# Optimization experiments

Hardware: AMD Instinct MI355X
Metric: run time of the kernel (lower is better)

The kernel has to match this reference:

```python
import jax, jax.numpy as jnp
import numpy as np

B, S, D = 8, 1024, 1024
H, K = 16, 64  # num_heads, key_dim
NEG_INF = -1e9  # Keras _large_compatible_negative for float32


def setup_inputs() -> dict:
    key = jax.random.key(0)
    ks = jax.random.split(key, 10)
    x = jax.random.normal(ks[0], (B, S, D), dtype=jnp.float32)
    mask = jax.random.bernoulli(ks[1], 0.9, (B, S))  # bool per-token mask
    w = lambda k, shp: (0.02 * jax.random.normal(k, shp, dtype=jnp.float32))
    return {
        "input_tensor": x,
        "input_mask": mask,
        "Wq": w(ks[2], (D, H, K)), "bq": jnp.zeros((H, K), jnp.float32),
        "Wk": w(ks[3], (D, H, K)), "bk": jnp.zeros((H, K), jnp.float32),
        "Wv": w(ks[4], (D, H, K)), "bv": jnp.zeros((H, K), jnp.float32),
        "Wo": w(ks[5], (H, K, D)), "bo": jnp.zeros((D,), jnp.float32),
    }


def reference(input_tensor, input_mask, Wq, bq, Wk, bk, Wv, bv, Wo, bo):
    x = input_tensor
    # QKV projections: [B,S,D] x [D,H,K] -> [B,S,H,K]
    q = jnp.einsum("bsd,dhk->bshk", x, Wq) + bq
    k = jnp.einsum("bsd,dhk->bshk", x, Wk) + bk
    v = jnp.einsum("bsd,dhk->bshk", x, Wv) + bv
    # scaled dot-product scores: [B,H,Sq,Sk]
    scores = jnp.einsum("bqhk,bshk->bhqs", q, k) / jnp.sqrt(
        jnp.asarray(K, x.dtype))
    # mask = logical_and(mask[...,None], mask[...,None,:]) per example
    m2 = (input_mask[:, :, None] & input_mask[:, None, :])  # [B,Sq,Sk]
    scores = scores + (1.0 - m2[:, None, :, :].astype(x.dtype)) * NEG_INF
    probs = jax.nn.softmax(scores, axis=-1)
    # attend and project out: [B,S,H,K] -> [B,S,D]
    ctx = jnp.einsum("bhqs,bshk->bqhk", probs, v)
    return jnp.einsum("bqhk,hkd->bqd", ctx, Wo) + bo
```

## Files before the change

### kernel.cpp

```cpp
#include <hip/hip_runtime.h>
#include <math.h>

#define Ss 1024
#define Dd 1024
#define Hh 16
#define Kk 64

typedef __bf16 bf16x8 __attribute__((ext_vector_type(8)));
typedef __bf16 bf16x4 __attribute__((ext_vector_type(4)));
typedef float  f32x4  __attribute__((ext_vector_type(4)));

#define MFMA16(a, b, c) __builtin_amdgcn_mfma_f32_16x16x32_bf16(a, b, c, 0, 0, 0)

typedef const __attribute__((address_space(1))) unsigned int* gas_ptr;
typedef __attribute__((address_space(3))) unsigned int* las_ptr;

__device__ __forceinline__ void async16(const void* g, void* l) {
    __builtin_amdgcn_global_load_lds((gas_ptr)g, (las_ptr)l, 16, 0, 0);
}

#define XB_E   8388608u
#define WT_E   3145728u
#define WOT_E  1048576u
#define QKV_E  8388608u

__global__ __launch_bounds__(256) void prep(
    const float* __restrict__ x,
    const float* __restrict__ Wq, const float* __restrict__ Wk,
    const float* __restrict__ Wv, const float* __restrict__ Wo,
    __bf16* __restrict__ xb, __bf16* __restrict__ WT, __bf16* __restrict__ WoT)
{
    __shared__ float tile[64][65];
    const int z = blockIdx.z;
    const int t = threadIdx.x;

    if (z == 4) {
        size_t blk = blockIdx.y * 16 + blockIdx.x;
        const float4* src = (const float4*)(x + blk * 32768);
        bf16x4* dst = (bf16x4*)(((__bf16*)xb) + blk * 32768);
        #pragma unroll
        for (int u = 0; u < 32; ++u) {
            float4 v = src[u * 256 + t];
            dst[u * 256 + t] =
                (bf16x4){(__bf16)v.x, (__bf16)v.y, (__bf16)v.z, (__bf16)v.w};
        }
        return;
    }

    const float* src = (z == 0) ? Wq : (z == 1) ? Wk : (z == 2) ? Wv : Wo;
    __bf16* dst = (z < 3) ? (WT + (size_t)z * 1048576) : WoT;

    int r0 = blockIdx.y * 64, c0 = blockIdx.x * 64;
    int rr = t >> 2, cg = (t & 3) * 16;

    #pragma unroll
    for (int u = 0; u < 4; ++u) {
        float4 v = *(const float4*)(src + (size_t)(r0 + rr) * 1024 + c0 + cg + u * 4);
        tile[rr][cg + u * 4 + 0] = v.x;
        tile[rr][cg + u * 4 + 1] = v.y;
        tile[rr][cg + u * 4 + 2] = v.z;
        tile[rr][cg + u * 4 + 3] = v.w;
    }
    __syncthreads();
    bf16x8 o0, o1;
    #pragma unroll
    for (int jj = 0; jj < 8; ++jj) o0[jj] = (__bf16)tile[cg + jj][rr];
    #pragma unroll
    for (int jj = 0; jj < 8; ++jj) o1[jj] = (__bf16)tile[cg + 8 + jj][rr];
    __bf16* dp = dst + (size_t)(c0 + rr) * 1024 + r0 + cg;
    *(bf16x8*)dp = o0;
    *(bf16x8*)(dp + 8) = o1;
}

__global__ __launch_bounds__(256) void gemm_bt(
    const __bf16* __restrict__ A, const __bf16* __restrict__ Bt, int mode,
    __bf16* __restrict__ qb, __bf16* __restrict__ kb, __bf16* __restrict__ vb,
    const float* __restrict__ bq, const float* __restrict__ bk,
    const float* __restrict__ bv,
    float* __restrict__ outf, const float* __restrict__ bo)
{
    __shared__ __align__(16) __bf16 As[128][32];
    __shared__ __align__(16) __bf16 Bs[128][32];

    const int t = threadIdx.x;
    const int wave = t >> 6, lane = t & 63;
    const int quad = lane >> 4, l16 = lane & 15;
    const int wm = wave >> 1, wn = wave & 1;
    const int m0 = blockIdx.y * 128, n0 = blockIdx.x * 128;

    const int sr = t >> 2;
    const int sc = (t & 3) * 8;

    f32x4 acc[4][4];
    #pragma unroll
    for (int i = 0; i < 4; ++i)
        #pragma unroll
        for (int j = 0; j < 4; ++j) acc[i][j] = (f32x4){0.f, 0.f, 0.f, 0.f};

    for (int k0 = 0; k0 < 1024; k0 += 32) {
        async16(A + (size_t)(m0 + sr) * 1024 + k0 + sc, &As[sr][sc]);
        async16(A + (size_t)(m0 + sr + 64) * 1024 + k0 + sc, &As[sr + 64][sc]);
        async16(Bt + (size_t)(n0 + sr) * 1024 + k0 + sc, &Bs[sr][sc]);
        async16(Bt + (size_t)(n0 + sr + 64) * 1024 + k0 + sc, &Bs[sr + 64][sc]);
        __syncthreads();

        bf16x8 af[4], bfr[4];
        #pragma unroll
        for (int i = 0; i < 4; ++i)
            af[i] = *(const bf16x8*)&As[wm * 64 + i * 16 + l16][quad * 8];
        #pragma unroll
        for (int j = 0; j < 4; ++j)
            bfr[j] = *(const bf16x8*)&Bs[wn * 64 + j * 16 + l16][quad * 8];
        #pragma unroll
        for (int i = 0; i < 4; ++i)
            #pragma unroll
            for (int j = 0; j < 4; ++j)
                acc[i][j] = MFMA16(af[i], bfr[j], acc[i][j]);
        __syncthreads();
    }

    if (mode == 0) {
        const int z = n0 >> 10;
        const float* bias = (z == 0) ? bq : (z == 1) ? bk : bv;
        const float sc2 = (z == 0) ? 0.125f : 1.0f;
        #pragma unroll
        for (int i = 0; i < 4; ++i) {
            int row = m0 + wm * 64 + i * 16 + quad * 4;
            int b = row >> 10, s = row & 1023;
            #pragma unroll
            for (int j = 0; j < 4; ++j) {
                int n1 = (n0 + wn * 64 + j * 16 + l16) & 1023;
                int h = n1 >> 6, ch = n1 & 63;
                float bia = bias[n1];
                if (z < 2) {
                    __bf16* dst = ((z == 0) ? qb : kb)
                        + ((size_t)(b * Hh + h) * Ss + s) * Kk + ch;
                    #pragma unroll
                    for (int r = 0; r < 4; ++r)
                        dst[(size_t)r * Kk] = (__bf16)((acc[i][j][r] + bia) * sc2);
                } else {
                    bf16x4 o;
                    #pragma unroll
                    for (int r = 0; r < 4; ++r) o[r] = (__bf16)(acc[i][j][r] + bia);
                    *(bf16x4*)(vb + ((size_t)(b * Hh + h) * Kk + ch) * Ss + s) = o;
                }
            }
        }
    } else {
        #pragma unroll
        for (int i = 0; i < 4; ++i) {
            int row = m0 + wm * 64 + i * 16 + quad * 4;
            #pragma unroll
            for (int j = 0; j < 4; ++j) {
                int n = n0 + wn * 64 + j * 16 + l16;
                float bia = bo[n];
                #pragma unroll
                for (int r = 0; r < 4; ++r)
                    outf[(size_t)(row + r) * 1024 + n] = acc[i][j][r] + bia;
            }
        }
    }
}

__global__ __launch_bounds__(256) void attn(
    const __bf16* __restrict__ qb, const __bf16* __restrict__ kb,
    const __bf16* __restrict__ vb, const int* __restrict__ mask,
    __bf16* __restrict__ ctx)
{
    const int bh = blockIdx.x;
    const int q0 = blockIdx.y * 128;
    const int b  = bh >> 4;
    const int h  = bh & 15;
    const size_t base = (size_t)bh * Ss * Kk;

    __shared__ __align__(16) __bf16 Qs[128][72];
    __shared__ __align__(16) __bf16 Ks[64][72];
    __shared__ __align__(16) __bf16 VTs[64][72];
    __shared__ __align__(16) __bf16 Ps[4][32][72];
    __shared__ float mkf[1024];

    const int t    = threadIdx.x;
    const int wave = t >> 6, lane = t & 63;
    const int quad = lane >> 4, l16 = lane & 15;
    const int qbase = wave * 32;

    #pragma unroll
    for (int p = 0; p < 4; ++p) {
        int idx = t + p * 256;
        int r = idx >> 3, g = idx & 7;
        *(bf16x8*)&Qs[r][g * 8] =
            *(const bf16x8*)(qb + base + (size_t)(q0 + r) * Kk + g * 8);
    }
    {
        int4 mi = *(const int4*)(mask + b * Ss + t * 4);
        mkf[t * 4 + 0] = (float)mi.x;
        mkf[t * 4 + 1] = (float)mi.y;
        mkf[t * 4 + 2] = (float)mi.z;
        mkf[t * 4 + 3] = (float)mi.w;
    }

    const int r0 = t >> 3, c0 = (t & 7) * 8;
    bf16x8 kr0, kr1, vr0, vr1;
    kr0 = *(const bf16x8*)(kb + base + (size_t)(r0) * Kk + c0);
    kr1 = *(const bf16x8*)(kb + base + (size_t)(r0 + 32) * Kk + c0);
    vr0 = *(const bf16x8*)(vb + base + (size_t)(r0) * Ss + c0);
    vr1 = *(const bf16x8*)(vb + base + (size_t)(r0 + 32) * Ss + c0);

    __syncthreads();

    bf16x8 aq[2][2];
    #pragma unroll
    for (int rg = 0; rg < 2; ++rg) {
        aq[rg][0] = *(const bf16x8*)&Qs[qbase + rg * 16 + l16][quad * 8];
        aq[rg][1] = *(const bf16x8*)&Qs[qbase + rg * 16 + l16][32 + quad * 8];
    }
    float mqf[2][4], omqf[2][4];
    #pragma unroll
    for (int rg = 0; rg < 2; ++rg)
        #pragma unroll
        for (int i = 0; i < 4; ++i) {
            float m = mkf[q0 + qbase + rg * 16 + quad * 4 + i];
            mqf[rg][i] = m; omqf[rg][i] = 1.0f - m;
        }

    f32x4 O[2][4];
    float lsum[2][4];
    #pragma unroll
    for (int rg = 0; rg < 2; ++rg)
        #pragma unroll
        for (int nb = 0; nb < 4; ++nb) O[rg][nb] = (f32x4){0.f, 0.f, 0.f, 0.f};
    #pragma unroll
    for (int rg = 0; rg < 2; ++rg)
        #pragma unroll
        for (int i = 0; i < 4; ++i) lsum[rg][i] = 0.f;

    for (int kt = 0; kt < Ss; kt += 64) {
        __syncthreads();
        *(bf16x8*)&Ks[r0][c0] = kr0;
        *(bf16x8*)&Ks[r0 + 32][c0] = kr1;
        *(bf16x8*)&VTs[r0][c0] = vr0;
        *(bf16x8*)&VTs[r0 + 32][c0] = vr1;
        __syncthreads();

        int ktn = kt + 64;
        if (ktn < Ss) {
            kr0 = *(const bf16x8*)(kb + base + (size_t)(ktn + r0) * Kk + c0);
            kr1 = *(const bf16x8*)(kb + base + (size_t)(ktn + r0 + 32) * Kk + c0);
            vr0 = *(const bf16x8*)(vb + base + (size_t)(r0) * Ss + ktn + c0);
            vr1 = *(const bf16x8*)(vb + base + (size_t)(r0 + 32) * Ss + ktn + c0);
        }

        float mkv[4];
        #pragma unroll
        for (int nb = 0; nb < 4; ++nb) mkv[nb] = mkf[kt + nb * 16 + l16];

        bf16x8 kb0[4], kb1[4];
        #pragma unroll
        for (int nb = 0; nb < 4; ++nb) {
            kb0[nb] = *(const bf16x8*)&Ks[nb * 16 + l16][quad * 8];
            kb1[nb] = *(const bf16x8*)&Ks[nb * 16 + l16][32 + quad * 8];
        }

        f32x4 s[2][4];
        #pragma unroll
        for (int rg = 0; rg < 2; ++rg)
            #pragma unroll
            for (int nb = 0; nb < 4; ++nb) {
                f32x4 a = (f32x4){0.f, 0.f, 0.f, 0.f};
                a = MFMA16(aq[rg][0], kb0[nb], a);
                a = MFMA16(aq[rg][1], kb1[nb], a);
                s[rg][nb] = a;
            }

        #pragma unroll
        for (int rg = 0; rg < 2; ++rg)
            #pragma unroll
            for (int i = 0; i < 4; ++i) {
                float ls = 0.f;
                #pragma unroll
                for (int nb = 0; nb < 4; ++nb) {
                    float p = __expf(s[rg][nb][i]) * mkv[nb];
                    p = p * mqf[rg][i] + omqf[rg][i];
                    Ps[wave][rg * 16 + quad * 4 + i][nb * 16 + l16] = (__bf16)p;
                    ls += p;
                }
                lsum[rg][i] += ls;
            }

        bf16x8 ap0[2], ap1[2];
        #pragma unroll
        for (int rg = 0; rg < 2; ++rg) {
            ap0[rg] = *(const bf16x8*)&Ps[wave][rg * 16 + l16][quad * 8];
            ap1[rg] = *(const bf16x8*)&Ps[wave][rg * 16 + l16][32 + quad * 8];
        }
        #pragma unroll
        for (int nb = 0; nb < 4; ++nb) {
            bf16x8 vb0 = *(const bf16x8*)&VTs[nb * 16 + l16][quad * 8];
            bf16x8 vb1 = *(const bf16x8*)&VTs[nb * 16 + l16][32 + quad * 8];
            #pragma unroll
            for (int rg = 0; rg < 2; ++rg) {
                O[rg][nb] = MFMA16(ap0[rg], vb0, O[rg][nb]);
                O[rg][nb] = MFMA16(ap1[rg], vb1, O[rg][nb]);
            }
        }
    }

    #pragma unroll
    for (int rg = 0; rg < 2; ++rg)
        #pragma unroll
        for (int i = 0; i < 4; ++i) {
            float l = lsum[rg][i];
            l += __shfl_xor(l, 1);
            l += __shfl_xor(l, 2);
            l += __shfl_xor(l, 4);
            l += __shfl_xor(l, 8);
            float inv = 1.0f / l;
            int srow = q0 + qbase + rg * 16 + quad * 4 + i;
            __bf16* dst = ctx + ((size_t)(b * Ss + srow) * Hh + h) * Kk;
            #pragma unroll
            for (int nb = 0; nb < 4; ++nb)
                dst[nb * 16 + l16] = (__bf16)(O[rg][nb][i] * inv);
        }
}

extern "C" void kernel_launch(void* const* d_in, const int* in_sizes, int n_in,
                              void* d_out, int out_size, void* d_ws, size_t ws_size,
                              hipStream_t stream) {
    const float* x    = (const float*)d_in[0];
    const int*   mask = (const int*)d_in[1];
    const float* Wq   = (const float*)d_in[2];
    const float* bq   = (const float*)d_in[3];
    const float* Wk   = (const float*)d_in[4];
    const float* bk   = (const float*)d_in[5];
    const float* Wv   = (const float*)d_in[6];
    const float* bv   = (const float*)d_in[7];
    const float* Wo   = (const float*)d_in[8];
    const float* bo   = (const float*)d_in[9];

    __bf16* xb   = (__bf16*)d_ws;
    __bf16* WT   = xb + XB_E;
    __bf16* WoT  = WT + WT_E;
    __bf16* qb   = WoT + WOT_E;
    __bf16* kb   = qb + QKV_E;
    __bf16* vb   = kb + QKV_E;
    __bf16* ctxb = vb + QKV_E;
    float* out = (float*)d_out;

    prep<<<dim3(16, 16, 5), 256, 0, stream>>>(x, Wq, Wk, Wv, Wo, xb, WT, WoT);
    gemm_bt<<<dim3(24, 64), 256, 0, stream>>>(xb, WT, 0, qb, kb, vb,
                                              bq, bk, bv, nullptr, nullptr);
    attn<<<dim3(128, 8), 256, 0, stream>>>(qb, kb, vb, mask, ctxb);
    gemm_bt<<<dim3(8, 64), 256, 0, stream>>>(ctxb, WoT, 1, nullptr, nullptr,
                                             nullptr, nullptr, nullptr, nullptr,
                                             out, bo);
}
```

Measured before the change: 275.9 us.

## Double-buffer GEMM tiles with register prefetch instead of direct global-to-LDS loads

Replaces the synchronous global_load_lds tile loads in the bf16 GEMM with a register-prefetch pipeline. The next K-slice is loaded into registers while MFMAs run on the current one, and LDS is double-buffered so only one barrier per iteration is needed. This aims to hide global memory latency behind compute, at the cost of extra VGPRs, doubled LDS, and an extra register-to-LDS store step.

New measurement: 271.7 us. No clear change (-1.5%).

```diff
diff --git a/kernel.cpp b/kernel.cpp
--- a/kernel.cpp
+++ b/kernel.cpp
@@ -11,13 +11,6 @@
 typedef float  f32x4  __attribute__((ext_vector_type(4)));
 
 #define MFMA16(a, b, c) __builtin_amdgcn_mfma_f32_16x16x32_bf16(a, b, c, 0, 0, 0)
-
-typedef const __attribute__((address_space(1))) unsigned int* gas_ptr;
-typedef __attribute__((address_space(3))) unsigned int* las_ptr;
-
-__device__ __forceinline__ void async16(const void* g, void* l) {
-    __builtin_amdgcn_global_load_lds((gas_ptr)g, (las_ptr)l, 16, 0, 0);
-}
 
 #define XB_E   8388608u
 #define WT_E   3145728u
@@ -79,8 +72,8 @@
     const float* __restrict__ bv,
     float* __restrict__ outf, const float* __restrict__ bo)
 {
-    __shared__ __align__(16) __bf16 As[128][32];
-    __shared__ __align__(16) __bf16 Bs[128][32];
+    __shared__ __align__(16) __bf16 As[2][128][32];
+    __shared__ __align__(16) __bf16 Bs[2][128][32];
 
     const int t = threadIdx.x;
     const int wave = t >> 6, lane = t & 63;
@@ -97,26 +90,44 @@
         #pragma unroll
         for (int j = 0; j < 4; ++j) acc[i][j] = (f32x4){0.f, 0.f, 0.f, 0.f};
 
+    const __bf16* pa0 = A + (size_t)(m0 + sr) * 1024 + sc;
+    const __bf16* pa1 = A + (size_t)(m0 + sr + 64) * 1024 + sc;
+    const __bf16* pb0 = Bt + (size_t)(n0 + sr) * 1024 + sc;
+    const __bf16* pb1 = Bt + (size_t)(n0 + sr + 64) * 1024 + sc;
+
+    bf16x8 ra0 = *(const bf16x8*)(pa0);
+    bf16x8 ra1 = *(const bf16x8*)(pa1);
+    bf16x8 rb0 = *(const bf16x8*)(pb0);
+    bf16x8 rb1 = *(const bf16x8*)(pb1);
+
     for (int k0 = 0; k0 < 1024; k0 += 32) {
-        async16(A + (size_t)(m0 + sr) * 1024 + k0 + sc, &As[sr][sc]);
-        async16(A + (size_t)(m0 + sr + 64) * 1024 + k0 + sc, &As[sr + 64][sc]);
-        async16(Bt + (size_t)(n0 + sr) * 1024 + k0 + sc, &Bs[sr][sc]);
-        async16(Bt + (size_t)(n0 + sr + 64) * 1024 + k0 + sc, &Bs[sr + 64][sc]);
+        const int p = (k0 >> 5) & 1;
+        *(bf16x8*)&As[p][sr][sc] = ra0;
+        *(bf16x8*)&As[p][sr + 64][sc] = ra1;
+        *(bf16x8*)&Bs[p][sr][sc] = rb0;
+        *(bf16x8*)&Bs[p][sr + 64][sc] = rb1;
         __syncthreads();
 
+        const int kn = k0 + 32;
+        if (kn < 1024) {
+            ra0 = *(const bf16x8*)(pa0 + kn);
+            ra1 = *(const bf16x8*)(pa1 + kn);
+            rb0 = *(const bf16x8*)(pb0 + kn);
+            rb1 = *(const bf16x8*)(pb1 + kn);
+        }
+
         bf16x8 af[4], bfr[4];
         #pragma unroll
         for (int i = 0; i < 4; ++i)
-            af[i] = *(const bf16x8*)&As[wm * 64 + i * 16 + l16][quad * 8];
+            af[i] = *(const bf16x8*)&As[p][wm * 64 + i * 16 + l16][quad * 8];
         #pragma unroll
         for (int j = 0; j < 4; ++j)
-            bfr[j] = *(const bf16x8*)&Bs[wn * 64 + j * 16 + l16][quad * 8];
+            bfr[j] = *(const bf16x8*)&Bs[p][wn * 64 + j * 16 + l16][quad * 8];
         #pragma unroll
         for (int i = 0; i < 4; ++i)
             #pragma unroll
             for (int j = 0; j < 4; ++j)
                 acc[i][j] = MFMA16(af[i], bfr[j], acc[i][j]);
-        __syncthreads();
     }
 
     if (mode == 0) {
```
